# Kernel optimization log

Measured on AMD Instinct MI355X. Metric: run time of the kernel, lower is better.

The kernel has to match this reference:

```python
import jax, jax.numpy as jnp
import numpy as np

HIDDEN = 1024
N_HEADS = 16
HEAD_DIM = 64
BS, QS = 4, 2048
NEG = -60000.0


def setup_inputs() -> dict:
    key = jax.random.key(0)
    k1, k2, k3, k4 = jax.random.split(key, 4)
    x = jax.random.normal(k1, (BS, QS, HIDDEN), dtype=jnp.float32)
    att_mask = jax.random.randint(k2, (BS, QS, QS), 0, 2).astype(bool)
    # nn.Linear(hidden, out, bias=False): store as [in, out] so y = x @ W
    W_qk = jax.random.normal(k3, (HIDDEN, 2 * N_HEADS * HEAD_DIM), dtype=jnp.float32) / np.sqrt(HIDDEN)
    W_v = jax.random.normal(k4, (HIDDEN, N_HEADS), dtype=jnp.float32) / np.sqrt(HIDDEN)
    return {"x": x, "att_mask": att_mask, "W_qk": W_qk, "W_v": W_v}


def reference(x, att_mask, W_qk, W_v):
    # mem is None -> c = x, ks == qs
    bs, qs, _ = x.shape
    n_heads = W_v.shape[1]
    head_dim = W_qk.shape[1] // (2 * n_heads)
    att_scale = 1.0 / head_dim ** 0.5

    qk = x @ W_qk                                   # [b, k, 2*n*d]
    query, key = jnp.split(qk, 2, axis=-1)
    value = x @ W_v                                 # [b, k, n]  (per-head V dim is 1)

    q = query.reshape(bs, qs, n_heads, head_dim)
    k = key.reshape(bs, qs, n_heads, head_dim)

    # att_score: [b, q, k, n]
    scores = jnp.einsum('bqnd,bknd->bqkn', q, k) * att_scale
    scores = jnp.where(att_mask[..., None], NEG, scores)  # True = masked
    prob = jax.nn.softmax(scores, axis=2)           # softmax over k
    # attended bqnd with d=1, then .sum(2) over heads -> [b, q, 1]
    attended = jnp.einsum('bqkn,bkn->bqn', prob, value)
    out = attended.sum(-1, keepdims=True)           # [b, q, 1]

    padded_mask = att_mask[:, -1]                   # [b, k] == [b, q]
    out = jnp.where(padded_mask[..., None], NEG, out)
    out = jax.nn.sigmoid(out)
    # torch version also returns out.nonzero() (data-dependent shape); omitted for jit.
    return out
```

## Files before the change

kernel.cpp:

```cpp
#include <hip/hip_runtime.h>

typedef unsigned short u16;
typedef unsigned int u32;
typedef unsigned long long u64;
typedef __attribute__((ext_vector_type(8))) short bf16x8;
typedef __attribute__((ext_vector_type(4))) float f32x4;

#define BATCH 4
#define SEQ 2048
#define HID 1024
#define NHEAD 16
#define HDIM 64
#define C1 0.18033688011112042f

#if __has_builtin(__builtin_amdgcn_exp2f)
#define EXP2(x) __builtin_amdgcn_exp2f(x)
#else
#define EXP2(x) exp2f(x)
#endif

__device__ __forceinline__ u16 f2bf(float f) {
    u32 u = __builtin_bit_cast(u32, f);
    u += 0x7fffu + ((u >> 16) & 1u);
    return (u16)(u >> 16);
}

__device__ __forceinline__ void gl_lds16(const void* g, void* l) {
    __builtin_amdgcn_global_load_lds((const __attribute__((address_space(1))) u32*)g,
                                     (__attribute__((address_space(3))) u32*)l, 16, 0, 0);
}

__global__ __launch_bounds__(1024) void flagk(const unsigned char* mask, int* flag) {
    __shared__ int any;
    if (threadIdx.x == 0) any = 0;
    __syncthreads();
    const uint4* m4 = (const uint4*)mask;
    u32 acc = 0;
#pragma unroll
    for (int j = 0; j < 4; ++j) {
        uint4 v = m4[threadIdx.x + j * 1024];
        acc |= (v.x | v.y | v.z | v.w) & 0xFFFFFF00u;
    }
    if (acc) atomicOr(&any, 1);
    __syncthreads();
    if (threadIdx.x == 0) *flag = (any == 0) ? 1 : 0;
}

__global__ void convx(const float* __restrict__ x, u16* __restrict__ xb) {
    int i = blockIdx.x * 256 + threadIdx.x;
    float4 v = ((const float4*)x)[i];
    ushort4 o;
    o.x = f2bf(v.x); o.y = f2bf(v.y); o.z = f2bf(v.z); o.w = f2bf(v.w);
    ((ushort4*)xb)[i] = o;
}

__global__ __launch_bounds__(256) void transw(const float* __restrict__ W, u16* __restrict__ wT) {
    __shared__ float t[32][33];
    int nb = blockIdx.x & 63, hb = blockIdx.x >> 6;
    int tx = threadIdx.x & 31, ty = threadIdx.x >> 5;
#pragma unroll
    for (int i = 0; i < 4; ++i)
        t[ty + i * 8][tx] = W[(size_t)(hb * 32 + ty + i * 8) * 2048 + nb * 32 + tx];
    __syncthreads();
#pragma unroll
    for (int i = 0; i < 4; ++i)
        wT[(size_t)(nb * 32 + ty + i * 8) * 1024 + hb * 32 + tx] = f2bf(t[tx][ty + i * 8]);
}

__global__ __launch_bounds__(256) void value_gemm(const float* __restrict__ x,
                                                  const float* __restrict__ Wv,
                                                  float* __restrict__ vT) {
    __shared__ float xs[16 * 1024];
    int s0 = blockIdx.x * 16;
    const float4* xg = (const float4*)(x + (size_t)s0 * HID);
    float4* xd = (float4*)xs;
    for (int i = threadIdx.x; i < 4096; i += 256) xd[i] = xg[i];
    __syncthreads();
    int sl = threadIdx.x >> 4, n = threadIdx.x & 15;
    float acc = 0.f;
    for (int hh = 0; hh < HID; ++hh) acc += xs[sl * HID + hh] * Wv[hh * 16 + n];
    int s = s0 + sl;
    int b = s >> 11, q = s & 2047;
    vT[((size_t)b * 16 + n) * SEQ + q] = acc;
}

__global__ void bitpack(const void* __restrict__ mask, const int* __restrict__ flag,
                        u64* __restrict__ bm) {
    int i = blockIdx.x * 256 + threadIdx.x;
    int v;
    if (*flag) v = ((const int*)mask)[i];
    else       v = ((const unsigned char*)mask)[i];
    u64 bits = __ballot(v == 0);
    if ((threadIdx.x & 63) == 0) bm[i >> 6] = bits;
}

__global__ __launch_bounds__(256) void proj_gemm(const u16* __restrict__ xb,
                                                 const u16* __restrict__ wT,
                                                 u16* __restrict__ qkb) {
    __shared__ __align__(16) u16 As[128 * 64];
    __shared__ __align__(16) u16 Bs[128 * 64];
    int tid = threadIdx.x, w = tid >> 6, lane = tid & 63;
    int bid = blockIdx.x;
    int swz = (bid & 7) * 128 + (bid >> 3);
    int bm = swz >> 4, bn = swz & 15;
    int m0 = bm * 128, n0 = bn * 128;
    int wm = w >> 1, wn = w & 1;
    f32x4 acc[4][4] = {};
    for (int kt = 0; kt < 16; ++kt) {
        int k0 = kt * 64;
        __syncthreads();
#pragma unroll
        for (int j = 0; j < 4; ++j) {
            int ci = (w * 4 + j) * 64 + lane;
            int row = ci >> 3, cp = ci & 7, cl = cp ^ (row & 7);
            gl_lds16(xb + (size_t)(m0 + row) * HID + k0 + cl * 8, &As[(w * 4 + j) * 512]);
            gl_lds16(wT + (size_t)(n0 + row) * HID + k0 + cl * 8, &Bs[(w * 4 + j) * 512]);
        }
        __syncthreads();
#pragma unroll
        for (int kk = 0; kk < 2; ++kk) {
            bf16x8 af[4], bf[4];
#pragma unroll
            for (int m = 0; m < 4; ++m) {
                int row = wm * 64 + m * 16 + (lane & 15);
                int cp = (kk * 4 + (lane >> 4)) ^ (row & 7);
                af[m] = *(const bf16x8*)&As[row * 64 + cp * 8];
            }
#pragma unroll
            for (int n = 0; n < 4; ++n) {
                int row = wn * 64 + n * 16 + (lane & 15);
                int cp = (kk * 4 + (lane >> 4)) ^ (row & 7);
                bf[n] = *(const bf16x8*)&Bs[row * 64 + cp * 8];
            }
#pragma unroll
            for (int m = 0; m < 4; ++m)
#pragma unroll
                for (int n = 0; n < 4; ++n)
                    acc[m][n] = __builtin_amdgcn_mfma_f32_16x16x32_bf16(af[m], bf[n], acc[m][n], 0, 0, 0);
        }
    }
    float scale = (bn < 8) ? C1 : 1.0f;
#pragma unroll
    for (int m = 0; m < 4; ++m)
#pragma unroll
        for (int n = 0; n < 4; ++n)
#pragma unroll
            for (int r = 0; r < 4; ++r) {
                int row = m0 + wm * 64 + m * 16 + (lane >> 4) * 4 + r;
                int col = n0 + wn * 64 + n * 16 + (lane & 15);
                qkb[(size_t)row * 2048 + col] = f2bf(acc[m][n][r] * scale);
            }
}

__global__ __launch_bounds__(512, 4) void attn(const u16* __restrict__ qkb,
                                               const float* __restrict__ vT,
                                               const u64* __restrict__ bmk,
                                               float* __restrict__ hatt) {
    __shared__ __align__(16) u16 Ks[3][64 * 64];
    __shared__ __align__(16) float Vh[2048];
    __shared__ __align__(16) float Tb[16][4];
    int tid = threadIdx.x, w = tid >> 6, lane = tid & 63;
    int g = lane >> 4, l15 = lane & 15, g4 = g * 4;
    int bid = blockIdx.x;
    int swzb = (bid & 7) * 64 + (bid >> 3);
    int qt = swzb & 7, h = (swzb >> 3) & 15, b = swzb >> 7;
    int q0 = qt * 256;
    if (tid < 64) Tb[tid >> 2][tid & 3] = (float)(((tid >> 2) >> (tid & 3)) & 1);
    int qA = q0 + w * 32 + l15, qB = qA + 16;
    const u16* qrowA = qkb + (size_t)(b * SEQ + qA) * 2048 + h * 64;
    const u16* qrowB = qkb + (size_t)(b * SEQ + qB) * 2048 + h * 64;
    bf16x8 qfA0 = *(const bf16x8*)(qrowA + g * 8);
    bf16x8 qfA1 = *(const bf16x8*)(qrowA + 32 + g * 8);
    bf16x8 qfB0 = *(const bf16x8*)(qrowB + g * 8);
    bf16x8 qfB1 = *(const bf16x8*)(qrowB + 32 + g * 8);
    gl_lds16(vT + ((size_t)b * 16 + h) * SEQ + tid * 4, &Vh[w * 256]);
    const u64* mrowA = bmk + ((size_t)b * SEQ + qA) * 32;
    const u64* mrowB = bmk + ((size_t)b * SEQ + qB) * 32;
    int srow = tid >> 3, scol = (tid & 7) ^ (srow & 7);
    const u16* ksrc = qkb + (size_t)(b * SEQ + srow) * 2048 + 1024 + h * 64 + scol * 8;
    u64 mA_cur = mrowA[0], mB_cur = mrowB[0];
    gl_lds16(ksrc, &Ks[0][w * 512]); ksrc += 64 * 2048;
    u64 mA_nxt = mrowA[1], mB_nxt = mrowB[1];
    gl_lds16(ksrc, &Ks[1][w * 512]); ksrc += 64 * 2048;
    int e0[4], e1[4];
#pragma unroll
    for (int cb = 0; cb < 4; ++cb) {
        int krow = cb * 16 + l15;
        e0[cb] = krow * 64 + ((g) ^ (krow & 7)) * 8;
        e1[cb] = krow * 64 + ((4 + g) ^ (krow & 7)) * 8;
    }
    float nmA0 = 0.f, nmA1 = 0.f, nmA2 = 0.f, nmA3 = 0.f;
    float dnA0 = 0.f, dnA1 = 0.f, dnA2 = 0.f, dnA3 = 0.f;
    float nmB0 = 0.f, nmB1 = 0.f, nmB2 = 0.f, nmB3 = 0.f;
    float dnB0 = 0.f, dnB1 = 0.f, dnB2 = 0.f, dnB3 = 0.f;
    asm volatile("s_waitcnt lgkmcnt(0)" ::: "memory");

    auto compute = [&](int kt) {
        const u16* kcur = &Ks[kt % 3][0];
        const float* vk = &Vh[kt * 64 + g4];
        u64 shA = mA_cur >> g4, shB = mB_cur >> g4;
        u32 aLo = (u32)shA, aHi = (u32)(shA >> 32);
        u32 bLo = (u32)shB, bHi = (u32)(shB >> 32);
        int idxA[4] = {(int)(aLo & 15), (int)((aLo >> 16) & 15),
                       (int)(aHi & 15), (int)((aHi >> 16) & 15)};
        int idxB[4] = {(int)(bLo & 15), (int)((bLo >> 16) & 15),
                       (int)(bHi & 15), (int)((bHi >> 16) & 15)};
#pragma unroll
        for (int cb = 0; cb < 4; ++cb) {
            bf16x8 kf0 = *(const bf16x8*)&kcur[e0[cb]];
            bf16x8 kf1 = *(const bf16x8*)&kcur[e1[cb]];
            f32x4 aA = {0.f, 0.f, 0.f, 0.f}, aB = {0.f, 0.f, 0.f, 0.f};
            aA = __builtin_amdgcn_mfma_f32_16x16x32_bf16(kf0, qfA0, aA, 0, 0, 0);
            aA = __builtin_amdgcn_mfma_f32_16x16x32_bf16(kf1, qfA1, aA, 0, 0, 0);
            aB = __builtin_amdgcn_mfma_f32_16x16x32_bf16(kf0, qfB0, aB, 0, 0, 0);
            aB = __builtin_amdgcn_mfma_f32_16x16x32_bf16(kf1, qfB1, aB, 0, 0, 0);
            const float4 mA4 = *(const float4*)&Tb[idxA[cb]][0];
            const float4 mB4 = *(const float4*)&Tb[idxB[cb]][0];
            const float4 vv = *(const float4*)&vk[cb * 16];
            float pA0 = EXP2(aA[0]) * mA4.x, pA1 = EXP2(aA[1]) * mA4.y;
            float pA2 = EXP2(aA[2]) * mA4.z, pA3 = EXP2(aA[3]) * mA4.w;
            float pB0 = EXP2(aB[0]) * mB4.x, pB1 = EXP2(aB[1]) * mB4.y;
            float pB2 = EXP2(aB[2]) * mB4.z, pB3 = EXP2(aB[3]) * mB4.w;
            dnA0 += pA0; dnA1 += pA1; dnA2 += pA2; dnA3 += pA3;
            dnB0 += pB0; dnB1 += pB1; dnB2 += pB2; dnB3 += pB3;
            nmA0 = fmaf(pA0, vv.x, nmA0); nmA1 = fmaf(pA1, vv.y, nmA1);
            nmA2 = fmaf(pA2, vv.z, nmA2); nmA3 = fmaf(pA3, vv.w, nmA3);
            nmB0 = fmaf(pB0, vv.x, nmB0); nmB1 = fmaf(pB1, vv.y, nmB1);
            nmB2 = fmaf(pB2, vv.z, nmB2); nmB3 = fmaf(pB3, vv.w, nmB3);
        }
    };

    for (int kt = 0; kt < 31; ++kt) {
        asm volatile("s_waitcnt vmcnt(3)" ::: "memory");
        __builtin_amdgcn_s_barrier();
        __builtin_amdgcn_sched_barrier(0);
        u64 mA_n2, mB_n2;
        if (kt < 30) {
            mA_n2 = mrowA[kt + 2]; mB_n2 = mrowB[kt + 2];
            gl_lds16(ksrc, &Ks[(kt + 2) % 3][w * 512]); ksrc += 64 * 2048;
        } else { mA_n2 = 0; mB_n2 = 0; }
        compute(kt);
        mA_cur = mA_nxt; mB_cur = mB_nxt;
        mA_nxt = mA_n2; mB_nxt = mB_n2;
    }
    asm volatile("s_waitcnt vmcnt(0)" ::: "memory");
    __builtin_amdgcn_s_barrier();
    __builtin_amdgcn_sched_barrier(0);
    compute(31);

    float numA = (nmA0 + nmA1) + (nmA2 + nmA3);
    float denA = (dnA0 + dnA1) + (dnA2 + dnA3);
    float numB = (nmB0 + nmB1) + (nmB2 + nmB3);
    float denB = (dnB0 + dnB1) + (dnB2 + dnB3);
    numA += __shfl_xor(numA, 16); denA += __shfl_xor(denA, 16);
    numA += __shfl_xor(numA, 32); denA += __shfl_xor(denA, 32);
    numB += __shfl_xor(numB, 16); denB += __shfl_xor(denB, 16);
    numB += __shfl_xor(numB, 32); denB += __shfl_xor(denB, 32);
    if (g == 0) {
        hatt[((size_t)b * SEQ + qA) * 16 + h] = numA / denA;
        hatt[((size_t)b * SEQ + qB) * 16 + h] = numB / denB;
    }
}

__global__ void epi(const float* __restrict__ hatt, const void* __restrict__ mask,
                    const int* __restrict__ flag, float* __restrict__ out) {
    int i = blockIdx.x * 256 + threadIdx.x;
    int b = i >> 11, q = i & 2047;
    const float4* hp = (const float4*)(hatt + (size_t)i * 16);
    float t = 0.f;
#pragma unroll
    for (int j = 0; j < 4; ++j) {
        float4 u = hp[j];
        t += u.x + u.y + u.z + u.w;
    }
    size_t mi = ((size_t)b * SEQ + (SEQ - 1)) * SEQ + q;
    int m;
    if (*flag) m = ((const int*)mask)[mi];
    else       m = ((const unsigned char*)mask)[mi];
    out[i] = m ? 0.f : 1.f / (1.f + expf(-t));
}

extern "C" void kernel_launch(void* const* d_in, const int* in_sizes, int n_in,
                              void* d_out, int out_size, void* d_ws, size_t ws_size,
                              hipStream_t stream) {
    const float* x = (const float*)d_in[0];
    const void* mask = d_in[1];
    const float* Wqk = (const float*)d_in[2];
    const float* Wv = (const float*)d_in[3];
    float* out = (float*)d_out;
    char* ws = (char*)d_ws;
    u16* xb = (u16*)(ws + 0);
    u16* wT = (u16*)(ws + 16777216);
    u16* qkb = (u16*)(ws + 20971520);
    float* vT = (float*)(ws + 54525952);
    u64* bm = (u64*)(ws + 55050240);
    float* hatt = (float*)(ws + 0);
    int* flag = (int*)(ws + 57147392);

    flagk<<<1, 1024, 0, stream>>>((const unsigned char*)mask, flag);
    convx<<<8192, 256, 0, stream>>>(x, xb);
    transw<<<2048, 256, 0, stream>>>(Wqk, wT);
    value_gemm<<<512, 256, 0, stream>>>(x, Wv, vT);
    bitpack<<<65536, 256, 0, stream>>>(mask, flag, bm);
    proj_gemm<<<1024, 256, 0, stream>>>(xb, wT, qkb);
    attn<<<512, 512, 0, stream>>>(qkb, vT, bm, hatt);
    epi<<<32, 256, 0, stream>>>(hatt, mask, flag, out);
}
```

Baseline: 176.6 us.

## Split attention key range in two blocks and combine partial sums in epilogue

The attention kernel now splits the key dimension into two halves, so twice as many blocks each process 16 key tiles instead of 32. Each block writes an unnormalized numerator/denominator pair, and the epilogue adds the two halves and divides. This is a split-K scheme meant to raise occupancy and fill more CUs with 1024 blocks instead of 512. In exchange it re-reads the Q fragments, writes twice as much intermediate data, and shortens the pipelined loop, which adds more prologue overhead per block. There is no max subtraction, so each half relies on the prescaled exp staying in range, the same as before.

```diff
diff --git a/kernel.cpp b/kernel.cpp
--- a/kernel.cpp
+++ b/kernel.cpp
@@ -157,14 +157,15 @@
                                                const u64* __restrict__ bmk,
                                                float* __restrict__ hatt) {
     __shared__ __align__(16) u16 Ks[3][64 * 64];
-    __shared__ __align__(16) float Vh[2048];
+    __shared__ __align__(16) float Vh[1024];
     __shared__ __align__(16) float Tb[16][4];
     int tid = threadIdx.x, w = tid >> 6, lane = tid & 63;
     int g = lane >> 4, l15 = lane & 15, g4 = g * 4;
     int bid = blockIdx.x;
-    int swzb = (bid & 7) * 64 + (bid >> 3);
-    int qt = swzb & 7, h = (swzb >> 3) & 15, b = swzb >> 7;
-    int q0 = qt * 256;
+    int bh = bid & 63, qtks = bid >> 6;
+    int ks = qtks & 1, qt = qtks >> 1;
+    int h = bh & 15, b = bh >> 4;
+    int q0 = qt * 256, kt0 = ks * 16;
     if (tid < 64) Tb[tid >> 2][tid & 3] = (float)(((tid >> 2) >> (tid & 3)) & 1);
     int qA = q0 + w * 32 + l15, qB = qA + 16;
     const u16* qrowA = qkb + (size_t)(b * SEQ + qA) * 2048 + h * 64;
@@ -173,11 +174,12 @@
     bf16x8 qfA1 = *(const bf16x8*)(qrowA + 32 + g * 8);
     bf16x8 qfB0 = *(const bf16x8*)(qrowB + g * 8);
     bf16x8 qfB1 = *(const bf16x8*)(qrowB + 32 + g * 8);
-    gl_lds16(vT + ((size_t)b * 16 + h) * SEQ + tid * 4, &Vh[w * 256]);
-    const u64* mrowA = bmk + ((size_t)b * SEQ + qA) * 32;
-    const u64* mrowB = bmk + ((size_t)b * SEQ + qB) * 32;
+    if (w < 4)
+        gl_lds16(vT + ((size_t)b * 16 + h) * SEQ + kt0 * 64 + tid * 4, &Vh[w * 256]);
+    const u64* mrowA = bmk + ((size_t)b * SEQ + qA) * 32 + kt0;
+    const u64* mrowB = bmk + ((size_t)b * SEQ + qB) * 32 + kt0;
     int srow = tid >> 3, scol = (tid & 7) ^ (srow & 7);
-    const u16* ksrc = qkb + (size_t)(b * SEQ + srow) * 2048 + 1024 + h * 64 + scol * 8;
+    const u16* ksrc = qkb + (size_t)(b * SEQ + kt0 * 64 + srow) * 2048 + 1024 + h * 64 + scol * 8;
     u64 mA_cur = mrowA[0], mB_cur = mrowB[0];
     gl_lds16(ksrc, &Ks[0][w * 512]); ksrc += 64 * 2048;
     u64 mA_nxt = mrowA[1], mB_nxt = mrowB[1];
@@ -195,9 +197,9 @@
     float dnB0 = 0.f, dnB1 = 0.f, dnB2 = 0.f, dnB3 = 0.f;
     asm volatile("s_waitcnt lgkmcnt(0)" ::: "memory");
 
-    auto compute = [&](int kt) {
-        const u16* kcur = &Ks[kt % 3][0];
-        const float* vk = &Vh[kt * 64 + g4];
+    auto compute = [&](int lt) {
+        const u16* kcur = &Ks[lt % 3][0];
+        const float* vk = &Vh[lt * 64 + g4];
         u64 shA = mA_cur >> g4, shB = mB_cur >> g4;
         u32 aLo = (u32)shA, aHi = (u32)(shA >> 32);
         u32 bLo = (u32)shB, bHi = (u32)(shB >> 32);
@@ -230,23 +232,23 @@
         }
     };
 
-    for (int kt = 0; kt < 31; ++kt) {
+    for (int lt = 0; lt < 15; ++lt) {
         asm volatile("s_waitcnt vmcnt(3)" ::: "memory");
         __builtin_amdgcn_s_barrier();
         __builtin_amdgcn_sched_barrier(0);
         u64 mA_n2, mB_n2;
-        if (kt < 30) {
-            mA_n2 = mrowA[kt + 2]; mB_n2 = mrowB[kt + 2];
-            gl_lds16(ksrc, &Ks[(kt + 2) % 3][w * 512]); ksrc += 64 * 2048;
+        if (lt < 14) {
+            mA_n2 = mrowA[lt + 2]; mB_n2 = mrowB[lt + 2];
+            gl_lds16(ksrc, &Ks[(lt + 2) % 3][w * 512]); ksrc += 64 * 2048;
         } else { mA_n2 = 0; mB_n2 = 0; }
-        compute(kt);
+        compute(lt);
         mA_cur = mA_nxt; mB_cur = mB_nxt;
         mA_nxt = mA_n2; mB_nxt = mB_n2;
     }
     asm volatile("s_waitcnt vmcnt(0)" ::: "memory");
     __builtin_amdgcn_s_barrier();
     __builtin_amdgcn_sched_barrier(0);
-    compute(31);
+    compute(15);
 
     float numA = (nmA0 + nmA1) + (nmA2 + nmA3);
     float denA = (dnA0 + dnA1) + (dnA2 + dnA3);
@@ -257,8 +259,9 @@
     numB += __shfl_xor(numB, 16); denB += __shfl_xor(denB, 16);
     numB += __shfl_xor(numB, 32); denB += __shfl_xor(denB, 32);
     if (g == 0) {
-        hatt[((size_t)b * SEQ + qA) * 16 + h] = numA / denA;
-        hatt[((size_t)b * SEQ + qB) * 16 + h] = numB / denB;
+        float2* o = (float2*)hatt;
+        o[(((size_t)b * SEQ + qA) * 16 + h) * 2 + ks] = make_float2(numA, denA);
+        o[(((size_t)b * SEQ + qB) * 16 + h) * 2 + ks] = make_float2(numB, denB);
     }
 }
 
@@ -266,12 +269,12 @@
                     const int* __restrict__ flag, float* __restrict__ out) {
     int i = blockIdx.x * 256 + threadIdx.x;
     int b = i >> 11, q = i & 2047;
-    const float4* hp = (const float4*)(hatt + (size_t)i * 16);
+    const float4* hp = (const float4*)(hatt + (size_t)i * 64);
     float t = 0.f;
 #pragma unroll
-    for (int j = 0; j < 4; ++j) {
+    for (int j = 0; j < 16; ++j) {
         float4 u = hp[j];
-        t += u.x + u.y + u.z + u.w;
+        t += (u.x + u.z) / (u.y + u.w);
     }
     size_t mi = ((size_t)b * SEQ + (SEQ - 1)) * SEQ + q;
     int m;
@@ -303,6 +306,6 @@
     value_gemm<<<512, 256, 0, stream>>>(x, Wv, vT);
     bitpack<<<65536, 256, 0, stream>>>(mask, flag, bm);
     proj_gemm<<<1024, 256, 0, stream>>>(xb, wT, qkb);
-    attn<<<512, 512, 0, stream>>>(qkb, vT, bm, hatt);
+    attn<<<1024, 512, 0, stream>>>(qkb, vT, bm, hatt);
     epi<<<32, 256, 0, stream>>>(hatt, mask, flag, out);
 }
```

Measured after the change: 185.0 us. 1.05x slower.

## Split attention into smaller 256-thread blocks and batch bitpack work per thread

Applied to the files above, without the earlier changes.

The attention kernel now launches 1024 blocks of 256 threads, each covering 128 queries instead of 256, so each thread issues two K-tile loads and two V loads per stage, with the wait count adjusted to match. All eight K fragments are read from LDS before the MFMA loop, so the LDS reads can overlap the matrix math. The bitpack kernel processes eight elements per thread with the flag read hoisted, cutting its grid eightfold. Smaller blocks raise the number of resident blocks but double K/V staging traffic per query. The earlier K fragment reads also raise register pressure.

```diff
diff --git a/kernel.cpp b/kernel.cpp
--- a/kernel.cpp
+++ b/kernel.cpp
@@ -86,12 +86,17 @@
 
 __global__ void bitpack(const void* __restrict__ mask, const int* __restrict__ flag,
                         u64* __restrict__ bm) {
-    int i = blockIdx.x * 256 + threadIdx.x;
-    int v;
-    if (*flag) v = ((const int*)mask)[i];
-    else       v = ((const unsigned char*)mask)[i];
-    u64 bits = __ballot(v == 0);
-    if ((threadIdx.x & 63) == 0) bm[i >> 6] = bits;
+    int base = blockIdx.x * 2048 + threadIdx.x;
+    int fl = *flag;
+#pragma unroll
+    for (int k = 0; k < 8; ++k) {
+        int i = base + k * 256;
+        int v;
+        if (fl) v = ((const int*)mask)[i];
+        else    v = ((const unsigned char*)mask)[i];
+        u64 bits = __ballot(v == 0);
+        if ((threadIdx.x & 63) == 0) bm[i >> 6] = bits;
+    }
 }
 
 __global__ __launch_bounds__(256) void proj_gemm(const u16* __restrict__ xb,
@@ -152,7 +157,7 @@
             }
 }
 
-__global__ __launch_bounds__(512, 4) void attn(const u16* __restrict__ qkb,
+__global__ __launch_bounds__(256, 4) void attn(const u16* __restrict__ qkb,
                                                const float* __restrict__ vT,
                                                const u64* __restrict__ bmk,
                                                float* __restrict__ hatt) {
@@ -162,10 +167,23 @@
     int tid = threadIdx.x, w = tid >> 6, lane = tid & 63;
     int g = lane >> 4, l15 = lane & 15, g4 = g * 4;
     int bid = blockIdx.x;
-    int swzb = (bid & 7) * 64 + (bid >> 3);
-    int qt = swzb & 7, h = (swzb >> 3) & 15, b = swzb >> 7;
-    int q0 = qt * 256;
+    int bh = bid & 63, qt = bid >> 6;
+    int h = bh & 15, b = bh >> 4;
+    int q0 = qt * 128;
     if (tid < 64) Tb[tid >> 2][tid & 3] = (float)(((tid >> 2) >> (tid & 3)) & 1);
+    const float* vsrc = vT + ((size_t)b * 16 + h) * SEQ;
+    gl_lds16(vsrc + (size_t)(0 * 256 + tid) * 4, &Vh[0 * 1024 + w * 256]);
+    gl_lds16(vsrc + (size_t)(1 * 256 + tid) * 4, &Vh[1 * 1024 + w * 256]);
+    int sr0 = tid >> 3, sc0 = (tid & 7) ^ (sr0 & 7);
+    int ci1 = 256 + tid, sr1 = ci1 >> 3, sc1 = (ci1 & 7) ^ (sr1 & 7);
+    const u16* ks0 = qkb + (size_t)(b * SEQ + sr0) * 2048 + 1024 + h * 64 + sc0 * 8;
+    const u16* ks1 = qkb + (size_t)(b * SEQ + sr1) * 2048 + 1024 + h * 64 + sc1 * 8;
+    gl_lds16(ks0, &Ks[0][w * 512]);
+    gl_lds16(ks1, &Ks[0][2048 + w * 512]);
+    ks0 += 64 * 2048; ks1 += 64 * 2048;
+    gl_lds16(ks0, &Ks[1][w * 512]);
+    gl_lds16(ks1, &Ks[1][2048 + w * 512]);
+    ks0 += 64 * 2048; ks1 += 64 * 2048;
     int qA = q0 + w * 32 + l15, qB = qA + 16;
     const u16* qrowA = qkb + (size_t)(b * SEQ + qA) * 2048 + h * 64;
     const u16* qrowB = qkb + (size_t)(b * SEQ + qB) * 2048 + h * 64;
@@ -173,15 +191,10 @@
     bf16x8 qfA1 = *(const bf16x8*)(qrowA + 32 + g * 8);
     bf16x8 qfB0 = *(const bf16x8*)(qrowB + g * 8);
     bf16x8 qfB1 = *(const bf16x8*)(qrowB + 32 + g * 8);
-    gl_lds16(vT + ((size_t)b * 16 + h) * SEQ + tid * 4, &Vh[w * 256]);
     const u64* mrowA = bmk + ((size_t)b * SEQ + qA) * 32;
     const u64* mrowB = bmk + ((size_t)b * SEQ + qB) * 32;
-    int srow = tid >> 3, scol = (tid & 7) ^ (srow & 7);
-    const u16* ksrc = qkb + (size_t)(b * SEQ + srow) * 2048 + 1024 + h * 64 + scol * 8;
     u64 mA_cur = mrowA[0], mB_cur = mrowB[0];
-    gl_lds16(ksrc, &Ks[0][w * 512]); ksrc += 64 * 2048;
     u64 mA_nxt = mrowA[1], mB_nxt = mrowB[1];
-    gl_lds16(ksrc, &Ks[1][w * 512]); ksrc += 64 * 2048;
     int e0[4], e1[4];
 #pragma unroll
     for (int cb = 0; cb < 4; ++cb) {
@@ -193,11 +206,18 @@
     float dnA0 = 0.f, dnA1 = 0.f, dnA2 = 0.f, dnA3 = 0.f;
     float nmB0 = 0.f, nmB1 = 0.f, nmB2 = 0.f, nmB3 = 0.f;
     float dnB0 = 0.f, dnB1 = 0.f, dnB2 = 0.f, dnB3 = 0.f;
+    asm volatile("s_waitcnt vmcnt(0)" ::: "memory");
     asm volatile("s_waitcnt lgkmcnt(0)" ::: "memory");
 
     auto compute = [&](int kt) {
         const u16* kcur = &Ks[kt % 3][0];
         const float* vk = &Vh[kt * 64 + g4];
+        bf16x8 kf[8];
+#pragma unroll
+        for (int cb = 0; cb < 4; ++cb) {
+            kf[cb * 2]     = *(const bf16x8*)&kcur[e0[cb]];
+            kf[cb * 2 + 1] = *(const bf16x8*)&kcur[e1[cb]];
+        }
         u64 shA = mA_cur >> g4, shB = mB_cur >> g4;
         u32 aLo = (u32)shA, aHi = (u32)(shA >> 32);
         u32 bLo = (u32)shB, bHi = (u32)(shB >> 32);
@@ -207,13 +227,11 @@
                        (int)(bHi & 15), (int)((bHi >> 16) & 15)};
 #pragma unroll
         for (int cb = 0; cb < 4; ++cb) {
-            bf16x8 kf0 = *(const bf16x8*)&kcur[e0[cb]];
-            bf16x8 kf1 = *(const bf16x8*)&kcur[e1[cb]];
             f32x4 aA = {0.f, 0.f, 0.f, 0.f}, aB = {0.f, 0.f, 0.f, 0.f};
-            aA = __builtin_amdgcn_mfma_f32_16x16x32_bf16(kf0, qfA0, aA, 0, 0, 0);
-            aA = __builtin_amdgcn_mfma_f32_16x16x32_bf16(kf1, qfA1, aA, 0, 0, 0);
-            aB = __builtin_amdgcn_mfma_f32_16x16x32_bf16(kf0, qfB0, aB, 0, 0, 0);
-            aB = __builtin_amdgcn_mfma_f32_16x16x32_bf16(kf1, qfB1, aB, 0, 0, 0);
+            aA = __builtin_amdgcn_mfma_f32_16x16x32_bf16(kf[cb * 2], qfA0, aA, 0, 0, 0);
+            aA = __builtin_amdgcn_mfma_f32_16x16x32_bf16(kf[cb * 2 + 1], qfA1, aA, 0, 0, 0);
+            aB = __builtin_amdgcn_mfma_f32_16x16x32_bf16(kf[cb * 2], qfB0, aB, 0, 0, 0);
+            aB = __builtin_amdgcn_mfma_f32_16x16x32_bf16(kf[cb * 2 + 1], qfB1, aB, 0, 0, 0);
             const float4 mA4 = *(const float4*)&Tb[idxA[cb]][0];
             const float4 mB4 = *(const float4*)&Tb[idxB[cb]][0];
             const float4 vv = *(const float4*)&vk[cb * 16];
@@ -231,13 +249,15 @@
     };
 
     for (int kt = 0; kt < 31; ++kt) {
-        asm volatile("s_waitcnt vmcnt(3)" ::: "memory");
+        asm volatile("s_waitcnt vmcnt(4)" ::: "memory");
         __builtin_amdgcn_s_barrier();
         __builtin_amdgcn_sched_barrier(0);
         u64 mA_n2, mB_n2;
         if (kt < 30) {
+            gl_lds16(ks0, &Ks[(kt + 2) % 3][w * 512]);
+            gl_lds16(ks1, &Ks[(kt + 2) % 3][2048 + w * 512]);
+            ks0 += 64 * 2048; ks1 += 64 * 2048;
             mA_n2 = mrowA[kt + 2]; mB_n2 = mrowB[kt + 2];
-            gl_lds16(ksrc, &Ks[(kt + 2) % 3][w * 512]); ksrc += 64 * 2048;
         } else { mA_n2 = 0; mB_n2 = 0; }
         compute(kt);
         mA_cur = mA_nxt; mB_cur = mB_nxt;
@@ -301,8 +321,8 @@
     convx<<<8192, 256, 0, stream>>>(x, xb);
     transw<<<2048, 256, 0, stream>>>(Wqk, wT);
     value_gemm<<<512, 256, 0, stream>>>(x, Wv, vT);
-    bitpack<<<65536, 256, 0, stream>>>(mask, flag, bm);
+    bitpack<<<8192, 256, 0, stream>>>(mask, flag, bm);
     proj_gemm<<<1024, 256, 0, stream>>>(xb, wT, qkb);
-    attn<<<512, 512, 0, stream>>>(qkb, vT, bm, hatt);
+    attn<<<1024, 256, 0, stream>>>(qkb, vT, bm, hatt);
     epi<<<32, 256, 0, stream>>>(hatt, mask, flag, out);
 }
```

Result: slower. 181.6 us (+2.8%).
